# Kernel optimization log

Measured on AMD Instinct MI355X. Metric: run time of the kernel, lower is better.

Reference implementation:

```python
import jax, jax.numpy as jnp
import numpy as np

D_IN = 2048
D_OUT = 2048
CTX = 2048
N_HEADS = 16
HEAD_DIM = D_OUT // N_HEADS
ROPE_BASE = 10000.0


def precompute_rope(head_dim, context_length, base=ROPE_BASE):
    inv_freq = 1.0 / (base ** (jnp.arange(0, head_dim, 2, dtype=jnp.float32) / head_dim))
    pos = jnp.arange(context_length, dtype=jnp.float32)
    angles = pos[:, None] * inv_freq[None, :]            # (ctx, head_dim/2)
    angles = jnp.concatenate([angles, angles], axis=-1)  # (ctx, head_dim)
    return jnp.cos(angles), jnp.sin(angles)


def compute_rope(x, cos, sin):
    # x: (b, h, s, d)
    s = x.shape[2]
    d = x.shape[3]
    x1, x2 = x[..., : d // 2], x[..., d // 2 :]
    rotated = jnp.concatenate([-x2, x1], axis=-1)
    c = cos[:s][None, None, :, :]
    sn = sin[:s][None, None, :, :]
    return x * c + rotated * sn


def setup_inputs() -> dict:
    key = jax.random.key(0)
    kx, kq, kk, kv, ko = jax.random.split(key, 5)
    scale = 1.0 / np.sqrt(D_IN)
    return {
        "x": jax.random.normal(kx, (2, 2048, D_IN), dtype=jnp.float32),
        "W_query": jax.random.normal(kq, (D_IN, D_OUT), dtype=jnp.float32) * scale,
        "W_key": jax.random.normal(kk, (D_IN, D_OUT), dtype=jnp.float32) * scale,
        "W_value": jax.random.normal(kv, (D_IN, D_OUT), dtype=jnp.float32) * scale,
        "W_out": jax.random.normal(ko, (D_OUT, D_OUT), dtype=jnp.float32) * scale,
    }


def reference(x, W_query, W_key, W_value, W_out):
    b, s, _ = x.shape
    cos, sin = precompute_rope(HEAD_DIM, CTX)

    def split_heads(t):
        return t.reshape(b, s, N_HEADS, HEAD_DIM).transpose(0, 2, 1, 3)  # (b,h,s,d)

    q = split_heads(x @ W_query)
    k = split_heads(x @ W_key)
    v = split_heads(x @ W_value)

    q = compute_rope(q, cos, sin)
    k = compute_rope(k, cos, sin)

    scores = jnp.einsum("bhqd,bhkd->bhqk", q, k) / jnp.sqrt(jnp.float32(HEAD_DIM))
    causal = jnp.tril(jnp.ones((s, s), dtype=bool))
    scores = jnp.where(causal[None, None], scores, -jnp.inf)
    attn = jax.nn.softmax(scores, axis=-1)

    ctx = jnp.einsum("bhqk,bhkd->bhqd", attn, v)
    ctx = ctx.transpose(0, 2, 1, 3).reshape(b, s, D_OUT)
    return ctx @ W_out
```

## Files before the change

kernel.cpp:

```cpp
#include <hip/hip_runtime.h>
#include <hip/hip_bf16.h>

typedef __attribute__((ext_vector_type(8))) short bf16x8;
typedef __attribute__((ext_vector_type(4))) float f32x4;
typedef __attribute__((ext_vector_type(16))) float f32x16;
typedef __attribute__((ext_vector_type(4))) unsigned int u32x4;

__device__ inline unsigned short f2bf(float f) {
    unsigned int u = __builtin_bit_cast(unsigned int, f);
    u += 0x7FFFu + ((u >> 16) & 1u);
    return (unsigned short)(u >> 16);
}
__device__ inline float bf2f(unsigned short h) {
    unsigned int u = ((unsigned int)h) << 16;
    return __builtin_bit_cast(float, u);
}
__device__ inline unsigned int pkbf(float a, float b) {
    return (unsigned int)f2bf(a) | ((unsigned int)f2bf(b) << 16);
}
__device__ inline unsigned int cvtpk(float lo, float hi) {
    unsigned int r;
    asm("v_cvt_pk_bf16_f32 %0, %1, %2" : "=v"(r) : "v"(lo), "v"(hi));
    return r;
}


__global__ void k_conv_x(const float* __restrict__ in, unsigned short* __restrict__ out, int n4) {
    int i = blockIdx.x * blockDim.x + threadIdx.x;
    if (i >= n4) return;
    float4 v = ((const float4*)in)[i];
    uint2 o;
    o.x = (unsigned)f2bf(v.x) | ((unsigned)f2bf(v.y) << 16);
    o.y = (unsigned)f2bf(v.z) | ((unsigned)f2bf(v.w) << 16);
    ((uint2*)out)[i] = o;
}

__global__ void k_wT(const float* __restrict__ w0, const float* __restrict__ w1,
                     const float* __restrict__ w2, const float* __restrict__ w3,
                     unsigned short* __restrict__ out) {
    __shared__ float tile[32][33];
    int z = blockIdx.z;
    const float* W = (z == 0) ? w0 : (z == 1) ? w1 : (z == 2) ? w2 : w3;
    unsigned short* O = out + (size_t)z * 2048 * 2048;
    int n0 = blockIdx.x * 32, k0 = blockIdx.y * 32;
    int tx = threadIdx.x & 31, ty = threadIdx.x >> 5;
#pragma unroll
    for (int j = 0; j < 4; ++j)
        tile[ty + j * 8][tx] = W[(size_t)(k0 + ty + j * 8) * 2048 + n0 + tx];
    __syncthreads();
#pragma unroll
    for (int j = 0; j < 4; ++j)
        O[(size_t)(n0 + ty + j * 8) * 2048 + k0 + tx] = f2bf(tile[tx][ty + j * 8]);
}

__global__ void k_rope_table(float* __restrict__ cosT, float* __restrict__ sinT) {
    int t = blockIdx.x * 256 + threadIdx.x;
    int s = t >> 6, i = t & 63;
    float inv = __expf(-((float)i / 64.0f) * 9.210340371976184f);
    float ang = (float)s * inv;
    cosT[t] = cosf(ang);
    sinT[t] = sinf(ang);
}

__global__ void k_rope_apply(unsigned short* qkv, const float* __restrict__ cosT,
                             const float* __restrict__ sinT) {
    int t = blockIdx.x * 256 + threadIdx.x;
    int i = t & 63, h = (t >> 6) & 15, s = (t >> 10) & 2047, b = t >> 21;
    float c = cosT[(s << 6) | i], sn = sinT[(s << 6) | i];
    size_t base = ((size_t)(b * 2048 + s)) * 2048 + h * 128 + i;
    const float SQ = 0.12751742f;
    {
        float a = bf2f(qkv[base]), bb = bf2f(qkv[base + 64]);
        qkv[base]      = f2bf((a * c - bb * sn) * SQ);
        qkv[base + 64] = f2bf((bb * c + a * sn) * SQ);
    }
    {
        size_t kbi = base + (size_t)8388608;
        float a = bf2f(qkv[kbi]), bb = bf2f(qkv[kbi + 64]);
        qkv[kbi]      = f2bf(a * c - bb * sn);
        qkv[kbi + 64] = f2bf(bb * c + a * sn);
    }
}

__global__ void k_vT(const unsigned short* __restrict__ V, unsigned short* __restrict__ VT) {
    __shared__ unsigned short tile[32][33];
    int z = blockIdx.z;
    int s0 = blockIdx.x * 32, d0 = blockIdx.y * 32;
    int b = z >> 4, h = z & 15;
    int tx = threadIdx.x & 31, ty = threadIdx.x >> 5;
#pragma unroll
    for (int j = 0; j < 4; ++j)
        tile[ty + j * 8][tx] =
            V[((size_t)(b * 2048 + s0 + ty + j * 8)) * 2048 + h * 128 + d0 + tx];
    __syncthreads();
#pragma unroll
    for (int j = 0; j < 4; ++j)
        VT[((size_t)(z * 128 + d0 + ty + j * 8)) * 2048 + s0 + tx] = tile[tx][ty + j * 8];
}

template <int OUT_MODE>
__global__ __launch_bounds__(256) void gemm_bt(const unsigned short* __restrict__ A,
                                               const unsigned short* __restrict__ Bt,
                                               void* __restrict__ outp, int M, int N, int K) {
    __shared__ __align__(16) unsigned short As[128 * 64];
    __shared__ __align__(16) unsigned short Bs[128 * 64];
    const int tid = threadIdx.x, w = tid >> 6, l = tid & 63;
    const int m0 = blockIdx.y * 128, n0 = blockIdx.x * 128;
    const int wm = w >> 1, wn = w & 1;
    const int l15 = l & 15, lq = l >> 4;
    f32x4 acc[4][4] = {};
    const int lr = l >> 3, lg = l & 7;
    const int srcg = lg ^ lr;

    const int nkt = K >> 6;
    for (int kt = 0; kt < nkt; ++kt) {
        if (kt) __syncthreads();
#pragma unroll
        for (int i = 0; i < 4; ++i) {
            int r0 = (w * 4 + i) * 8;
            int row = r0 + lr;
            const unsigned short* sa = A + (size_t)(m0 + row) * K + kt * 64 + srcg * 8;
            __builtin_amdgcn_global_load_lds((const void*)sa, (void*)&As[(w * 4 + i) * 512], 16, 0, 0);
            const unsigned short* sb = Bt + (size_t)(n0 + row) * K + kt * 64 + srcg * 8;
            __builtin_amdgcn_global_load_lds((const void*)sb, (void*)&Bs[(w * 4 + i) * 512], 16, 0, 0);
        }
        __syncthreads();
#pragma unroll
        for (int kb = 0; kb < 2; ++kb) {
            bf16x8 af[4], bfr[4];
#pragma unroll
            for (int mi = 0; mi < 4; ++mi) {
                int row = wm * 64 + mi * 16 + l15;
                int g = (kb * 4 + lq) ^ (row & 7);
                af[mi] = *(const bf16x8*)&As[row * 64 + g * 8];
            }
#pragma unroll
            for (int ni = 0; ni < 4; ++ni) {
                int row = wn * 64 + ni * 16 + l15;
                int g = (kb * 4 + lq) ^ (row & 7);
                bfr[ni] = *(const bf16x8*)&Bs[row * 64 + g * 8];
            }
#pragma unroll
            for (int mi = 0; mi < 4; ++mi)
#pragma unroll
                for (int ni = 0; ni < 4; ++ni)
                    acc[mi][ni] = __builtin_amdgcn_mfma_f32_16x16x32_bf16(af[mi], bfr[ni],
                                                                          acc[mi][ni], 0, 0, 0);
        }
    }

    if constexpr (OUT_MODE == 0) {
        int tsel = n0 >> 11, nloc = n0 & 2047;
        unsigned short* op = (unsigned short*)outp + (size_t)tsel * M * 2048;
#pragma unroll
        for (int mi = 0; mi < 4; ++mi)
#pragma unroll
            for (int ni = 0; ni < 4; ++ni)
#pragma unroll
                for (int r = 0; r < 4; ++r) {
                    int row = m0 + wm * 64 + mi * 16 + lq * 4 + r;
                    int col = nloc + wn * 64 + ni * 16 + l15;
                    op[(size_t)row * 2048 + col] = f2bf(acc[mi][ni][r]);
                }
    } else {
        float* op = (float*)outp;
#pragma unroll
        for (int mi = 0; mi < 4; ++mi)
#pragma unroll
            for (int ni = 0; ni < 4; ++ni)
#pragma unroll
                for (int r = 0; r < 4; ++r) {
                    int row = m0 + wm * 64 + mi * 16 + lq * 4 + r;
                    int col = n0 + wn * 64 + ni * 16 + l15;
                    op[(size_t)row * 2048 + col] = acc[mi][ni][r];
                }
    }
}

__global__ __launch_bounds__(256, 2) void k_attn(const unsigned short* __restrict__ Qp,
                                                 const unsigned short* __restrict__ Kp,
                                                 const unsigned short* __restrict__ VTp,
                                                 unsigned short* __restrict__ ctx) {
    __shared__ __align__(16) unsigned short Ks[2][64 * 128];
    __shared__ __align__(16) unsigned short Vs[2][128 * 64];
    const int tid = threadIdx.x, w = tid >> 6, l = tid & 63;
    const int l31 = l & 31, hi = l >> 5;
    const int x = blockIdx.x, bh = x & 31, pr = x >> 5;
    const int b = bh >> 4, h = bh & 15;
    const size_t b2048 = (size_t)b * 2048;
    const int h128 = h * 128;
    const size_t bh128 = (size_t)bh * 128;

    auto stage = [&](int kv) {
        const int bsel = kv & 1;
        const size_t kvoff = (size_t)kv * 64;
#pragma unroll
        for (int i = 0; i < 4; ++i) {
            int gi = w * 256 + i * 64 + l;
            int row = gi >> 4, g = gi & 15;
            int sg = g ^ (row & 7);
            const unsigned short* src = Kp + (b2048 + kvoff + row) * 2048 + h128 + sg * 8;
            __builtin_amdgcn_global_load_lds((const void*)src,
                                             (void*)&Ks[bsel][w * 2048 + i * 512], 16, 0, 0);
        }
#pragma unroll
        for (int i = 0; i < 4; ++i) {
            int gi = w * 256 + i * 64 + l;
            int row = gi >> 3, g = gi & 7;
            int sg = g ^ (row & 7);
            const unsigned short* src = VTp + (bh128 + row) * 2048 + kvoff + sg * 8;
            __builtin_amdgcn_global_load_lds((const void*)src,
                                             (void*)&Vs[bsel][w * 2048 + i * 512], 16, 0, 0);
        }
    };

    for (int pi = 0; pi < 2; ++pi) {
        const int t = pi ? pr : (15 - pr);
        const int q0 = t * 128;
        const int wrow0 = q0 + w * 32;
        const int qg = wrow0 + l31;

        bf16x8 qf[8];
        {
            const unsigned short* qb = Qp + (b2048 + qg) * 2048 + h128 + hi * 8;
#pragma unroll
            for (int ds = 0; ds < 8; ++ds) qf[ds] = *(const bf16x8*)(qb + ds * 16);
#pragma unroll
            for (int ds = 0; ds < 8; ++ds) asm volatile("" ::"v"(qf[ds]));
        }
        f32x16 Oa[4] = {};
        float m2 = -1e30f, l2 = 0.f;
        const int kvmax = 2 * t + 1;

        stage(0);
        for (int kv = 0; kv <= kvmax; ++kv) {
            const int cur = kv & 1;
            if (kv < kvmax) {
                stage(kv + 1);
                asm volatile("s_waitcnt vmcnt(8)" ::: "memory");
            } else {
                asm volatile("s_waitcnt vmcnt(0)" ::: "memory");
            }
            __builtin_amdgcn_s_barrier();
            __builtin_amdgcn_sched_barrier(0);

            const int kvb = kv * 64;
            if (kvb <= wrow0 + 31) {
                f32x16 S[2] = {};
                __builtin_amdgcn_s_setprio(1);
#pragma unroll
                for (int ds = 0; ds < 8; ++ds)
#pragma unroll
                    for (int st = 0; st < 2; ++st) {
                        int row = st * 32 + l31;
                        int g = (ds * 2 + hi) ^ (row & 7);
                        bf16x8 kf = *(const bf16x8*)&Ks[cur][row * 128 + g * 8];
                        S[st] = __builtin_amdgcn_mfma_f32_32x32x16_bf16(kf, qf[ds], S[st], 0, 0, 0);
                    }
                __builtin_amdgcn_s_setprio(0);

                if (kvb + 63 > wrow0) {
#pragma unroll
                    for (int st = 0; st < 2; ++st)
#pragma unroll
                        for (int r = 0; r < 16; ++r) {
                            int kpos = kvb + st * 32 + (r & 3) + 8 * (r >> 2) + 4 * hi;
                            if (kpos > qg) S[st][r] = -1e30f;
                        }
                }

                float pmax = -1e30f;
#pragma unroll
                for (int st = 0; st < 2; ++st)
#pragma unroll
                    for (int r = 0; r < 16; ++r) pmax = fmaxf(pmax, S[st][r]);
                pmax = fmaxf(pmax, __shfl_xor(pmax, 32));
                if (__any(pmax > m2 + 8.0f)) {
                    float mn = fmaxf(m2, pmax);
                    float sc = __builtin_amdgcn_exp2f(m2 - mn);
                    m2 = mn;
                    l2 *= sc;
#pragma unroll
                    for (int dt = 0; dt < 4; ++dt)
#pragma unroll
                        for (int e = 0; e < 16; ++e) Oa[dt][e] *= sc;
                }
                float rs = 0.f;
#pragma unroll
                for (int st = 0; st < 2; ++st)
#pragma unroll
                    for (int r = 0; r < 16; ++r) {
                        float p = __builtin_amdgcn_exp2f(S[st][r] - m2);
                        S[st][r] = p;
                        rs += p;
                    }
                rs += __shfl_xor(rs, 32);
                l2 += rs;

                bf16x8 pfrag[4];
#pragma unroll
                for (int ks = 0; ks < 4; ++ks) {
                    const int st = ks >> 1, base = (ks & 1) * 8;
                    unsigned int x0 = cvtpk(S[st][base + 0], S[st][base + 1]);
                    unsigned int x1 = cvtpk(S[st][base + 2], S[st][base + 3]);
                    unsigned int y0 = cvtpk(S[st][base + 4], S[st][base + 5]);
                    unsigned int y1 = cvtpk(S[st][base + 6], S[st][base + 7]);
                    unsigned int t0 = hi ? x0 : y0, t1 = hi ? x1 : y1;
                    t0 = (unsigned int)__shfl_xor((int)t0, 32);
                    t1 = (unsigned int)__shfl_xor((int)t1, 32);
                    u32x4 fw;
                    fw.x = hi ? t0 : x0;
                    fw.y = hi ? t1 : x1;
                    fw.z = hi ? y0 : t0;
                    fw.w = hi ? y1 : t1;
                    pfrag[ks] = __builtin_bit_cast(bf16x8, fw);
                }

                __builtin_amdgcn_s_setprio(1);
#pragma unroll
                for (int ks = 0; ks < 4; ++ks)
#pragma unroll
                    for (int dt = 0; dt < 4; ++dt) {
                        int row = dt * 32 + l31;
                        int g = (ks * 2 + hi) ^ (row & 7);
                        bf16x8 vf = *(const bf16x8*)&Vs[cur][row * 64 + g * 8];
                        Oa[dt] = __builtin_amdgcn_mfma_f32_32x32x16_bf16(vf, pfrag[ks], Oa[dt], 0, 0, 0);
                    }
                __builtin_amdgcn_s_setprio(0);
            }
            __builtin_amdgcn_sched_barrier(0);
            __builtin_amdgcn_s_barrier();
        }

        float inv = 1.0f / l2;
        unsigned short* cb = ctx + (b2048 + qg) * 2048 + h128;
#pragma unroll
        for (int dt = 0; dt < 4; ++dt)
#pragma unroll
            for (int g = 0; g < 4; ++g) {
                uint2 pv;
                pv.x = cvtpk(Oa[dt][4 * g + 0] * inv, Oa[dt][4 * g + 1] * inv);
                pv.y = cvtpk(Oa[dt][4 * g + 2] * inv, Oa[dt][4 * g + 3] * inv);
                *(uint2*)(cb + dt * 32 + 8 * g + 4 * hi) = pv;
            }
    }
}


extern "C" void kernel_launch(void* const* d_in, const int* in_sizes, int n_in,
                              void* d_out, int out_size, void* d_ws, size_t ws_size,
                              hipStream_t stream) {
    const float* x  = (const float*)d_in[0];
    const float* wq = (const float*)d_in[1];
    const float* wk = (const float*)d_in[2];
    const float* wv = (const float*)d_in[3];
    const float* wo = (const float*)d_in[4];

    char* ws = (char*)d_ws;
    unsigned short* xb  = (unsigned short*)(ws);
    unsigned short* wT  = (unsigned short*)(ws + 16777216);
    unsigned short* qkv = (unsigned short*)(ws + 50331648);
    unsigned short* vT  = (unsigned short*)(ws + 100663296);
    float* cosT = (float*)(ws + 117440512);
    float* sinT = (float*)(ws + 117964800);
    unsigned short* ctx = xb;

    k_conv_x<<<8192, 256, 0, stream>>>(x, xb, 2097152);
    k_wT<<<dim3(64, 64, 4), 256, 0, stream>>>(wq, wk, wv, wo, wT);
    k_rope_table<<<512, 256, 0, stream>>>(cosT, sinT);
    gemm_bt<0><<<dim3(48, 32), 256, 0, stream>>>(xb, wT, (void*)qkv, 4096, 6144, 2048);
    k_rope_apply<<<16384, 256, 0, stream>>>(qkv, cosT, sinT);
    k_vT<<<dim3(64, 4, 32), 256, 0, stream>>>(qkv + 2 * 8388608, vT);
    k_attn<<<256, 256, 0, stream>>>(qkv, qkv + 8388608, vT, ctx);
    gemm_bt<1><<<dim3(16, 32), 256, 0, stream>>>(ctx, wT + (size_t)3 * 4194304, d_out,
                                                 4096, 2048, 2048);
}
```

Measured before the change: 264.7 us.

## Fuse RoPE and V transpose into the QKV GEMM epilogue

```diff
diff --git a/kernel.cpp b/kernel.cpp
--- a/kernel.cpp
+++ b/kernel.cpp
@@ -53,55 +53,21 @@
         O[(size_t)(n0 + ty + j * 8) * 2048 + k0 + tx] = f2bf(tile[tx][ty + j * 8]);
 }
 
-__global__ void k_rope_table(float* __restrict__ cosT, float* __restrict__ sinT) {
+__global__ void k_cs_table(float2* __restrict__ csT) {
     int t = blockIdx.x * 256 + threadIdx.x;
     int s = t >> 6, i = t & 63;
     float inv = __expf(-((float)i / 64.0f) * 9.210340371976184f);
     float ang = (float)s * inv;
-    cosT[t] = cosf(ang);
-    sinT[t] = sinf(ang);
-}
-
-__global__ void k_rope_apply(unsigned short* qkv, const float* __restrict__ cosT,
-                             const float* __restrict__ sinT) {
-    int t = blockIdx.x * 256 + threadIdx.x;
-    int i = t & 63, h = (t >> 6) & 15, s = (t >> 10) & 2047, b = t >> 21;
-    float c = cosT[(s << 6) | i], sn = sinT[(s << 6) | i];
-    size_t base = ((size_t)(b * 2048 + s)) * 2048 + h * 128 + i;
-    const float SQ = 0.12751742f;
-    {
-        float a = bf2f(qkv[base]), bb = bf2f(qkv[base + 64]);
-        qkv[base]      = f2bf((a * c - bb * sn) * SQ);
-        qkv[base + 64] = f2bf((bb * c + a * sn) * SQ);
-    }
-    {
-        size_t kbi = base + (size_t)8388608;
-        float a = bf2f(qkv[kbi]), bb = bf2f(qkv[kbi + 64]);
-        qkv[kbi]      = f2bf(a * c - bb * sn);
-        qkv[kbi + 64] = f2bf(bb * c + a * sn);
-    }
-}
-
-__global__ void k_vT(const unsigned short* __restrict__ V, unsigned short* __restrict__ VT) {
-    __shared__ unsigned short tile[32][33];
-    int z = blockIdx.z;
-    int s0 = blockIdx.x * 32, d0 = blockIdx.y * 32;
-    int b = z >> 4, h = z & 15;
-    int tx = threadIdx.x & 31, ty = threadIdx.x >> 5;
-#pragma unroll
-    for (int j = 0; j < 4; ++j)
-        tile[ty + j * 8][tx] =
-            V[((size_t)(b * 2048 + s0 + ty + j * 8)) * 2048 + h * 128 + d0 + tx];
-    __syncthreads();
-#pragma unroll
-    for (int j = 0; j < 4; ++j)
-        VT[((size_t)(z * 128 + d0 + ty + j * 8)) * 2048 + s0 + tx] = tile[tx][ty + j * 8];
+    csT[t] = make_float2(cosf(ang), sinf(ang));
 }
 
 template <int OUT_MODE>
 __global__ __launch_bounds__(256) void gemm_bt(const unsigned short* __restrict__ A,
                                                const unsigned short* __restrict__ Bt,
-                                               void* __restrict__ outp, int M, int N, int K) {
+                                               void* __restrict__ outp,
+                                               unsigned short* __restrict__ vtp,
+                                               const float2* __restrict__ csT,
+                                               int M, int N, int K) {
     __shared__ __align__(16) unsigned short As[128 * 64];
     __shared__ __align__(16) unsigned short Bs[128 * 64];
     const int tid = threadIdx.x, w = tid >> 6, l = tid & 63;
@@ -136,7 +102,7 @@
             }
 #pragma unroll
             for (int ni = 0; ni < 4; ++ni) {
-                int row = wn * 64 + ni * 16 + l15;
+                int row = wn * 32 + (ni & 1) * 16 + (ni >> 1) * 64 + l15;
                 int g = (kb * 4 + lq) ^ (row & 7);
                 bfr[ni] = *(const bf16x8*)&Bs[row * 64 + g * 8];
             }
@@ -150,8 +116,42 @@
     }
 
     if constexpr (OUT_MODE == 0) {
-        int tsel = n0 >> 11, nloc = n0 & 2047;
-        unsigned short* op = (unsigned short*)outp + (size_t)tsel * M * 2048;
+        const int tsel = n0 >> 11, nloc = n0 & 2047;
+        if (tsel < 2) {
+            unsigned short* op = (unsigned short*)outp + (size_t)tsel * M * 2048;
+            const float scale = (tsel == 0) ? 0.12751742f : 1.0f;
+#pragma unroll
+            for (int mi = 0; mi < 4; ++mi)
+#pragma unroll
+                for (int ni = 0; ni < 2; ++ni) {
+                    const int i = wn * 32 + ni * 16 + l15;
+#pragma unroll
+                    for (int r = 0; r < 4; ++r) {
+                        int row = m0 + wm * 64 + mi * 16 + lq * 4 + r;
+                        int sp = row & 2047;
+                        float2 cs = csT[sp * 64 + i];
+                        float a = acc[mi][ni][r], bb = acc[mi][ni + 2][r];
+                        op[(size_t)row * 2048 + nloc + i]      = f2bf((a * cs.x - bb * cs.y) * scale);
+                        op[(size_t)row * 2048 + nloc + i + 64] = f2bf((bb * cs.x + a * cs.y) * scale);
+                    }
+                }
+        } else {
+            const int h = nloc >> 7;
+            const int bsel = m0 >> 11;
+            const int sp0 = (m0 & 2047) + wm * 64;
+#pragma unroll
+            for (int mi = 0; mi < 4; ++mi)
+#pragma unroll
+                for (int ni = 0; ni < 4; ++ni) {
+                    int d = wn * 32 + (ni & 1) * 16 + (ni >> 1) * 64 + l15;
+                    uint2 pv;
+                    pv.x = cvtpk(acc[mi][ni][0], acc[mi][ni][1]);
+                    pv.y = cvtpk(acc[mi][ni][2], acc[mi][ni][3]);
+                    *(uint2*)&vtp[((size_t)((bsel * 16 + h) * 128 + d)) * 2048 + sp0 + mi * 16 + lq * 4] = pv;
+                }
+        }
+    } else {
+        float* op = (float*)outp;
 #pragma unroll
         for (int mi = 0; mi < 4; ++mi)
 #pragma unroll
@@ -159,19 +159,7 @@
 #pragma unroll
                 for (int r = 0; r < 4; ++r) {
                     int row = m0 + wm * 64 + mi * 16 + lq * 4 + r;
-                    int col = nloc + wn * 64 + ni * 16 + l15;
-                    op[(size_t)row * 2048 + col] = f2bf(acc[mi][ni][r]);
-                }
-    } else {
-        float* op = (float*)outp;
-#pragma unroll
-        for (int mi = 0; mi < 4; ++mi)
-#pragma unroll
-            for (int ni = 0; ni < 4; ++ni)
-#pragma unroll
-                for (int r = 0; r < 4; ++r) {
-                    int row = m0 + wm * 64 + mi * 16 + lq * 4 + r;
-                    int col = n0 + wn * 64 + ni * 16 + l15;
+                    int col = n0 + wn * 32 + (ni & 1) * 16 + (ni >> 1) * 64 + l15;
                     op[(size_t)row * 2048 + col] = acc[mi][ni][r];
                 }
     }
@@ -361,17 +349,14 @@
     unsigned short* wT  = (unsigned short*)(ws + 16777216);
     unsigned short* qkv = (unsigned short*)(ws + 50331648);
     unsigned short* vT  = (unsigned short*)(ws + 100663296);
-    float* cosT = (float*)(ws + 117440512);
-    float* sinT = (float*)(ws + 117964800);
+    float2* csT = (float2*)(ws + 117440512);
     unsigned short* ctx = xb;
 
     k_conv_x<<<8192, 256, 0, stream>>>(x, xb, 2097152);
     k_wT<<<dim3(64, 64, 4), 256, 0, stream>>>(wq, wk, wv, wo, wT);
-    k_rope_table<<<512, 256, 0, stream>>>(cosT, sinT);
-    gemm_bt<0><<<dim3(48, 32), 256, 0, stream>>>(xb, wT, (void*)qkv, 4096, 6144, 2048);
-    k_rope_apply<<<16384, 256, 0, stream>>>(qkv, cosT, sinT);
-    k_vT<<<dim3(64, 4, 32), 256, 0, stream>>>(qkv + 2 * 8388608, vT);
+    k_cs_table<<<512, 256, 0, stream>>>(csT);
+    gemm_bt<0><<<dim3(48, 32), 256, 0, stream>>>(xb, wT, (void*)qkv, vT, csT, 4096, 6144, 2048);
     k_attn<<<256, 256, 0, stream>>>(qkv, qkv + 8388608, vT, ctx);
-    gemm_bt<1><<<dim3(16, 32), 256, 0, stream>>>(ctx, wT + (size_t)3 * 4194304, d_out,
+    gemm_bt<1><<<dim3(16, 32), 256, 0, stream>>>(ctx, wT + (size_t)3 * 4194304, d_out, vT, csT,
                                                  4096, 2048, 2048);
 }
```

New measurement: 248.6 us. 6.1% less time.
